# Kernel optimization log

Measured on AMD Instinct MI355X. Metric: run time of the kernel, lower is better.

The kernel has to match this reference:

```python
import jax, jax.numpy as jnp
import numpy as np

EMBED_DIM = 2048
NUM_Q_HEADS = 16
HEAD_DIM = EMBED_DIM // NUM_Q_HEADS  # 128
SCALE = 1.0 / np.sqrt(EMBED_DIM)     # note: module uses 1/sqrt(embed_dim)
B, S = 4, 2048


def setup_inputs() -> dict:
    key = jax.random.key(0)
    ks = jax.random.split(key, 9)
    sd = 0.02
    return {
        "x": jax.random.normal(ks[0], (B, S, EMBED_DIM), dtype=jnp.float32),
        "Wq": jax.random.normal(ks[1], (EMBED_DIM, EMBED_DIM), dtype=jnp.float32) * sd,
        "bq": jnp.zeros((EMBED_DIM,), dtype=jnp.float32),
        "Wk": jax.random.normal(ks[2], (HEAD_DIM, EMBED_DIM), dtype=jnp.float32) * sd,
        "bk": jnp.zeros((HEAD_DIM,), dtype=jnp.float32),
        "Wv": jax.random.normal(ks[3], (HEAD_DIM, EMBED_DIM), dtype=jnp.float32) * sd,
        "bv": jnp.zeros((HEAD_DIM,), dtype=jnp.float32),
        "Wo": jax.random.normal(ks[4], (EMBED_DIM, EMBED_DIM), dtype=jnp.float32) * sd,
        "bo": jnp.zeros((EMBED_DIM,), dtype=jnp.float32),
    }


def reference(x, Wq, bq, Wk, bk, Wv, bv, Wo, bo):
    b, s, _ = x.shape
    # projections (nn.Linear: y = x @ W.T + b)
    q = (x @ Wq.T + bq).reshape(b, s, NUM_Q_HEADS, HEAD_DIM)  # [b,s,h,d]
    k = x @ Wk.T + bk   # [b,t,d] single KV head (MQA)
    v = x @ Wv.T + bv   # [b,t,d]
    # SDPA with single K/V head broadcast across all query heads
    scores = jnp.einsum("bshd,btd->bhst", q, k) * SCALE  # [b,h,s,t]
    attn = jax.nn.softmax(scores, axis=-1)
    out = jnp.einsum("bhst,btd->bshd", attn, v).reshape(b, s, EMBED_DIM)
    return out @ Wo.T + bo
```

## Files before the change

kernel.cpp:

```cpp
#include <hip/hip_runtime.h>
#include <stdint.h>
#include <cmath>

#define B_ 4
#define S_ 2048
#define E_ 2048
#define H_ 16
#define D_ 128
#define M_ (B_*S_)

typedef unsigned short u16;
typedef __attribute__((ext_vector_type(8))) short short8;
typedef __attribute__((ext_vector_type(4))) float f32x4;

__device__ __forceinline__ u16 f2bf(float f) {
  union { float f; uint32_t u; } v; v.f = f;
  uint32_t r = v.u + 0x7fffu + ((v.u >> 16) & 1u);
  return (u16)(r >> 16);
}

__device__ __forceinline__ float exp2_fast(float x) {
  float r; asm("v_exp_f32 %0, %1" : "=v"(r) : "v"(x)); return r;
}

__device__ __forceinline__ uint32_t cvtpk_bf16(float lo, float hi) {
  uint32_t r; asm("v_cvt_pk_bf16_f32 %0, %1, %2" : "=v"(r) : "v"(lo), "v"(hi));
  return r;
}

__device__ __forceinline__ void async16(const void* g, void* s) {
  __builtin_amdgcn_global_load_lds(
      (const __attribute__((address_space(1))) uint32_t*)g,
      (__attribute__((address_space(3))) uint32_t*)s, 16, 0, 0);
}

#define XSEG   4194304L
#define WQSEG  1048576L
#define WKSEG    65536L
__global__ __launch_bounds__(256) void cvt_all(
    const float4* __restrict__ x,  const float4* __restrict__ wq,
    const float4* __restrict__ wk, const float4* __restrict__ wv,
    const float4* __restrict__ wo,
    ushort4* __restrict__ xb,  ushort4* __restrict__ wqb,
    ushort4* __restrict__ wkb, ushort4* __restrict__ wvb,
    ushort4* __restrict__ wob) {
  long i = (long)blockIdx.x * 256 + threadIdx.x;
  const float4* src; ushort4* dst; long off;
  if (i < XSEG)                            { src = x;  dst = xb;  off = 0; }
  else if (i < XSEG + WQSEG)               { src = wq; dst = wqb; off = XSEG; }
  else if (i < XSEG + WQSEG + WKSEG)       { src = wk; dst = wkb; off = XSEG + WQSEG; }
  else if (i < XSEG + WQSEG + 2*WKSEG)     { src = wv; dst = wvb; off = XSEG + WQSEG + WKSEG; }
  else                                     { src = wo; dst = wob; off = XSEG + WQSEG + 2*WKSEG; }
  long j = i - off;
  float4 v = src[j];
  ushort4 o;
  o.x = f2bf(v.x); o.y = f2bf(v.y); o.z = f2bf(v.z); o.w = f2bf(v.w);
  dst[j] = o;
}

template<int OUT>
__global__ __launch_bounds__(512, 2) void gemm256(
    const u16* __restrict__ A, const u16* __restrict__ Bm,
    const float* __restrict__ bias, void* __restrict__ Cout,
    int Ndim, int K, float oscale) {
  __shared__ u16 lA[2][256*64];
  __shared__ u16 lB[2][256*64];
  const int tid = threadIdx.x;
  const int l = tid & 63, w = tid >> 6;
  const int lr = l & 15, lg = l >> 4;
  const int wm = w >> 2, wn = w & 3;
  const int row0A = blockIdx.y * 256;
  const int row0B = blockIdx.x * 256;

  f32x4 acc[8][4] = {};

  auto STAGE = [&](int d, int k0) {
    #pragma unroll
    for (int c = 0; c < 4; ++c) {
      int idx = c*512 + tid;
      int r = idx >> 3, ch = idx & 7;
      async16(A + (size_t)(row0A + r)*K + k0 + (ch ^ (r & 7))*8,
              &lA[d][(size_t)(c*512 + w*64)*8]);
    }
    #pragma unroll
    for (int c = 0; c < 4; ++c) {
      int idx = c*512 + tid;
      int r = idx >> 3, ch = idx & 7;
      async16(Bm + (size_t)(row0B + r)*K + k0 + (ch ^ (r & 7))*8,
              &lB[d][(size_t)(c*512 + w*64)*8]);
    }
  };

  STAGE(0, 0);
  STAGE(1, 64);
  asm volatile("s_waitcnt vmcnt(8)" ::: "memory");
  __builtin_amdgcn_s_barrier();
  asm volatile("" ::: "memory");

  const int nk = K >> 6;
  for (int k = 0; k < nk; ++k) {
    const int d = k & 1;
    const char* bA = (const char*)&lA[d][0];
    const char* bB = (const char*)&lB[d][0];
    short8 afr[8][2], bfr[4][2];

    #pragma unroll
    for (int i = 0; i < 4; ++i)
      #pragma unroll
      for (int ks = 0; ks < 2; ++ks) {
        int ra = wm*128 + i*16 + lr;
        afr[i][ks] = *(const short8*)(bA + ((ra*128 + ks*64 + lg*16) ^ ((ra & 7) << 4)));
      }
    #pragma unroll
    for (int j = 0; j < 2; ++j)
      #pragma unroll
      for (int ks = 0; ks < 2; ++ks) {
        int rb = wn*64 + j*16 + lr;
        bfr[j][ks] = *(const short8*)(bB + ((rb*128 + ks*64 + lg*16) ^ ((rb & 7) << 4)));
      }
    __builtin_amdgcn_s_barrier();
    asm volatile("" ::: "memory");
    __builtin_amdgcn_s_setprio(1);
    #pragma unroll
    for (int i = 0; i < 4; ++i)
      #pragma unroll
      for (int j = 0; j < 2; ++j)
        #pragma unroll
        for (int ks = 0; ks < 2; ++ks)
          acc[i][j] = __builtin_amdgcn_mfma_f32_16x16x32_bf16(
                        afr[i][ks], bfr[j][ks], acc[i][j], 0, 0, 0);
    __builtin_amdgcn_s_setprio(0);
    __builtin_amdgcn_s_barrier();
    asm volatile("" ::: "memory");

    #pragma unroll
    for (int j = 2; j < 4; ++j)
      #pragma unroll
      for (int ks = 0; ks < 2; ++ks) {
        int rb = wn*64 + j*16 + lr;
        bfr[j][ks] = *(const short8*)(bB + ((rb*128 + ks*64 + lg*16) ^ ((rb & 7) << 4)));
      }
    __builtin_amdgcn_s_barrier();
    asm volatile("" ::: "memory");
    __builtin_amdgcn_s_setprio(1);
    #pragma unroll
    for (int i = 0; i < 4; ++i)
      #pragma unroll
      for (int j = 2; j < 4; ++j)
        #pragma unroll
        for (int ks = 0; ks < 2; ++ks)
          acc[i][j] = __builtin_amdgcn_mfma_f32_16x16x32_bf16(
                        afr[i][ks], bfr[j][ks], acc[i][j], 0, 0, 0);
    __builtin_amdgcn_s_setprio(0);
    __builtin_amdgcn_s_barrier();
    asm volatile("" ::: "memory");

    #pragma unroll
    for (int i = 4; i < 8; ++i)
      #pragma unroll
      for (int ks = 0; ks < 2; ++ks) {
        int ra = wm*128 + i*16 + lr;
        afr[i][ks] = *(const short8*)(bA + ((ra*128 + ks*64 + lg*16) ^ ((ra & 7) << 4)));
      }
    __builtin_amdgcn_s_barrier();
    asm volatile("" ::: "memory");
    __builtin_amdgcn_s_setprio(1);
    #pragma unroll
    for (int i = 4; i < 8; ++i)
      #pragma unroll
      for (int j = 0; j < 2; ++j)
        #pragma unroll
        for (int ks = 0; ks < 2; ++ks)
          acc[i][j] = __builtin_amdgcn_mfma_f32_16x16x32_bf16(
                        afr[i][ks], bfr[j][ks], acc[i][j], 0, 0, 0);
    __builtin_amdgcn_s_setprio(0);
    __builtin_amdgcn_s_barrier();
    asm volatile("" ::: "memory");

    bool st = (k + 2 < nk);
    if (st) STAGE(d, (k + 2) << 6);
    __builtin_amdgcn_s_barrier();
    asm volatile("" ::: "memory");
    __builtin_amdgcn_s_setprio(1);
    #pragma unroll
    for (int i = 4; i < 8; ++i)
      #pragma unroll
      for (int j = 2; j < 4; ++j)
        #pragma unroll
        for (int ks = 0; ks < 2; ++ks)
          acc[i][j] = __builtin_amdgcn_mfma_f32_16x16x32_bf16(
                        afr[i][ks], bfr[j][ks], acc[i][j], 0, 0, 0);
    __builtin_amdgcn_s_setprio(0);
    if (st) asm volatile("s_waitcnt vmcnt(8)" ::: "memory");
    else    asm volatile("s_waitcnt vmcnt(0)" ::: "memory");
    __builtin_amdgcn_s_barrier();
    asm volatile("" ::: "memory");
  }

  const int crow0 = row0A + wm*128;
  const int ccol0 = row0B + wn*64;
  #pragma unroll
  for (int j = 0; j < 4; ++j) {
    int col = ccol0 + j*16 + lr;
    float bv = bias[col];
    #pragma unroll
    for (int i = 0; i < 8; ++i) {
      #pragma unroll
      for (int r = 0; r < 4; ++r) {
        int row = crow0 + i*16 + lg*4 + r;
        float vo = (acc[i][j][r] + bv) * oscale;
        if (OUT == 0) ((float*)Cout)[(size_t)row*Ndim + col] = vo;
        else          ((u16*)Cout)[(size_t)row*Ndim + col] = f2bf(vo);
      }
    }
  }
}

__global__ __launch_bounds__(256) void gemm_kv(
    const u16* __restrict__ A, const u16* __restrict__ Wkb, const u16* __restrict__ Wvb,
    const float* __restrict__ bkp, const float* __restrict__ bvp,
    u16* __restrict__ kout, u16* __restrict__ vTout) {
  __shared__ u16 lA[128*64];
  __shared__ u16 lB[128*64];
  const int tid = threadIdx.x;
  const int l = tid & 63, w = tid >> 6;
  const int lr = l & 15, lg = l >> 4;
  const int wr = w >> 1, wc = w & 1;
  const int row0A = blockIdx.y * 128;
  const bool isV = (blockIdx.x != 0);
  const u16* Bm = isV ? Wvb : Wkb;
  const float* bias = isV ? bvp : bkp;

  f32x4 acc[4][4] = {};

  for (int k0 = 0; k0 < E_; k0 += 64) {
    __syncthreads();
    #pragma unroll
    for (int c = 0; c < 4; ++c) {
      int idx = c*256 + tid;
      int r = idx >> 3, ch = idx & 7;
      async16(A + (size_t)(row0A + r)*E_ + k0 + (ch ^ (r & 7))*8,
              lA + (size_t)(c*256 + w*64)*8);
    }
    #pragma unroll
    for (int c = 0; c < 4; ++c) {
      int idx = c*256 + tid;
      int r = idx >> 3, ch = idx & 7;
      async16(Bm + (size_t)r*E_ + k0 + (ch ^ (r & 7))*8,
              lB + (size_t)(c*256 + w*64)*8);
    }
    __syncthreads();
    #pragma unroll
    for (int ks = 0; ks < 2; ++ks) {
      short8 af[4], bfr[4];
      #pragma unroll
      for (int i = 0; i < 4; ++i) {
        int ra = wr*64 + i*16 + lr;
        af[i] = *(const short8*)((const char*)lA +
                 ((ra*128 + ks*64 + lg*16) ^ ((ra & 7) << 4)));
        int rb = wc*64 + i*16 + lr;
        bfr[i] = *(const short8*)((const char*)lB +
                 ((rb*128 + ks*64 + lg*16) ^ ((rb & 7) << 4)));
      }
      #pragma unroll
      for (int i = 0; i < 4; ++i)
        #pragma unroll
        for (int j = 0; j < 4; ++j)
          acc[i][j] = __builtin_amdgcn_mfma_f32_16x16x32_bf16(
                        af[i], bfr[j], acc[i][j], 0, 0, 0);
    }
  }

  const int crow0 = row0A + wr*64;
  #pragma unroll
  for (int j = 0; j < 4; ++j) {
    int col = wc*64 + j*16 + lr;
    float bvv = bias[col];
    #pragma unroll
    for (int i = 0; i < 4; ++i) {
      #pragma unroll
      for (int r = 0; r < 4; ++r) {
        int row = crow0 + i*16 + lg*4 + r;
        float vo = acc[i][j][r] + bvv;
        if (isV) vTout[(size_t)col*M_ + row] = f2bf(vo);
        else     kout[(size_t)row*D_ + col] = f2bf(vo);
      }
    }
  }
}

__global__ __launch_bounds__(512) void mqa_flash(
    const u16* __restrict__ q, const u16* __restrict__ k,
    const u16* __restrict__ vT, u16* __restrict__ o) {
  __shared__ u16 lKbuf[2][64*128];
  __shared__ u16 lVbuf[2][128*64];

  const int tid = threadIdx.x;
  const int l = tid & 63, w = tid >> 6;
  const int lr = l & 15, lg = l >> 4;
  const int qt = blockIdx.x, b = blockIdx.z;
  const int h = blockIdx.y*2 + (w >> 2);
  const int qrow0 = b*S_ + qt*128 + (w & 3)*32;

  short8 qf[2][4];
  #pragma unroll
  for (int st = 0; st < 2; ++st) {
    const u16* qp = q + (size_t)(qrow0 + st*16 + lr)*E_ + h*D_;
    #pragma unroll
    for (int ks = 0; ks < 4; ++ks)
      qf[st][ks] = *(const short8*)(qp + ks*32 + lg*8);
  }

  short8 ones;
  #pragma unroll
  for (int j = 0; j < 8; ++j) ones[j] = (short)0x3F80;

  f32x4 oa[2][8];
  f32x4 la[2] = {f32x4{0.f,0.f,0.f,0.f}, f32x4{0.f,0.f,0.f,0.f}};
  #pragma unroll
  for (int st = 0; st < 2; ++st)
    #pragma unroll
    for (int dn = 0; dn < 8; ++dn) oa[st][dn] = f32x4{0.f,0.f,0.f,0.f};

  const u16* kbase = k + (size_t)b*S_*D_;
  const u16* vbase = vT + (size_t)b*S_;
  char* lK0 = (char*)&lKbuf[0][0];
  char* lV0 = (char*)&lVbuf[0][0];

  auto STAGE = [&](int off, int tt) {
    #pragma unroll
    for (int c = 0; c < 2; ++c) {
      int idx = c*512 + tid;
      int s = idx >> 4, ch = idx & 15;
      int pr = (s & 32) | ((s & 12) << 1) | ((s & 16) >> 2) | (s & 3);
      async16(kbase + (size_t)(tt + pr)*D_ + (ch ^ (s & 7))*8,
              lK0 + off + (size_t)(c*512 + w*64)*16);
    }
    #pragma unroll
    for (int c = 0; c < 2; ++c) {
      int idx = c*512 + tid;
      int r = idx >> 3, ch = idx & 7;
      async16(vbase + (size_t)r*M_ + tt + (ch ^ (r & 7))*8,
              lV0 + off + (size_t)(c*512 + w*64)*16);
    }
  };

  STAGE(0, 0);
  __syncthreads();
  int roff = 0;

  for (int t0 = 0; t0 < S_; t0 += 64) {
    const int woff = roff ^ 16384;
    if (t0 + 64 < S_) STAGE(woff, t0 + 64);

    const char* lKc = lK0 + roff;
    const char* lVc = lV0 + roff;

    f32x4 sa[2][4];
    #pragma unroll
    for (int st = 0; st < 2; ++st)
      #pragma unroll
      for (int n = 0; n < 4; ++n) sa[st][n] = f32x4{0.f,0.f,0.f,0.f};
    __builtin_amdgcn_s_setprio(1);
    #pragma unroll
    for (int n = 0; n < 4; ++n)
      #pragma unroll
      for (int ks = 0; ks < 4; ++ks) {
        short8 kf = *(const short8*)(lKc +
                    (((n*16 + lr)*256 + ks*64 + lg*16) ^ ((lr & 7) << 4)));
        sa[0][n] = __builtin_amdgcn_mfma_f32_16x16x32_bf16(kf, qf[0][ks], sa[0][n], 0, 0, 0);
        sa[1][n] = __builtin_amdgcn_mfma_f32_16x16x32_bf16(kf, qf[1][ks], sa[1][n], 0, 0, 0);
      }
    __builtin_amdgcn_s_setprio(0);

    short8 pa[2][2];
    #pragma unroll
    for (int st = 0; st < 2; ++st) {
      #pragma unroll
      for (int n = 0; n < 4; ++n)
        #pragma unroll
        for (int r = 0; r < 4; ++r)
          sa[st][n][r] = exp2_fast(sa[st][n][r]);
      #pragma unroll
      for (int ks = 0; ks < 2; ++ks) {
        union { short8 s8; uint32_t u[4]; } pu;
        pu.u[0] = cvtpk_bf16(sa[st][2*ks  ][0], sa[st][2*ks  ][1]);
        pu.u[1] = cvtpk_bf16(sa[st][2*ks  ][2], sa[st][2*ks  ][3]);
        pu.u[2] = cvtpk_bf16(sa[st][2*ks+1][0], sa[st][2*ks+1][1]);
        pu.u[3] = cvtpk_bf16(sa[st][2*ks+1][2], sa[st][2*ks+1][3]);
        pa[st][ks] = pu.s8;
      }
    }

    __builtin_amdgcn_s_setprio(1);
    la[0] = __builtin_amdgcn_mfma_f32_16x16x32_bf16(pa[0][0], ones, la[0], 0, 0, 0);
    la[0] = __builtin_amdgcn_mfma_f32_16x16x32_bf16(pa[0][1], ones, la[0], 0, 0, 0);
    la[1] = __builtin_amdgcn_mfma_f32_16x16x32_bf16(pa[1][0], ones, la[1], 0, 0, 0);
    la[1] = __builtin_amdgcn_mfma_f32_16x16x32_bf16(pa[1][1], ones, la[1], 0, 0, 0);

    #pragma unroll
    for (int dn = 0; dn < 8; ++dn)
      #pragma unroll
      for (int ks = 0; ks < 2; ++ks) {
        short8 vf = *(const short8*)(lVc +
                    (((dn*16 + lr)*128 + ks*64 + lg*16) ^ ((lr & 7) << 4)));
        oa[0][dn] = __builtin_amdgcn_mfma_f32_16x16x32_bf16(pa[0][ks], vf, oa[0][dn], 0, 0, 0);
        oa[1][dn] = __builtin_amdgcn_mfma_f32_16x16x32_bf16(pa[1][ks], vf, oa[1][dn], 0, 0, 0);
      }
    __builtin_amdgcn_s_setprio(0);

    __syncthreads();
    roff = woff;
  }

  #pragma unroll
  for (int st = 0; st < 2; ++st) {
    #pragma unroll
    for (int r = 0; r < 4; ++r) {
      float inv = 1.0f / la[st][r];
      u16* orow = o + (size_t)(qrow0 + st*16 + lg*4 + r)*E_ + h*D_ + lr;
      #pragma unroll
      for (int dn = 0; dn < 8; ++dn)
        orow[dn*16] = f2bf(oa[st][dn][r] * inv);
    }
  }
}

extern "C" void kernel_launch(void* const* d_in, const int* in_sizes, int n_in,
                              void* d_out, int out_size, void* d_ws, size_t ws_size,
                              hipStream_t stream) {
  (void)in_sizes; (void)n_in; (void)out_size; (void)ws_size;
  const float* x  = (const float*)d_in[0];
  const float* Wq = (const float*)d_in[1];
  const float* bq = (const float*)d_in[2];
  const float* Wk = (const float*)d_in[3];
  const float* bk = (const float*)d_in[4];
  const float* Wv = (const float*)d_in[5];
  const float* bv = (const float*)d_in[6];
  const float* Wo = (const float*)d_in[7];
  const float* bo = (const float*)d_in[8];
  float* out = (float*)d_out;

  char* ws = (char*)d_ws;
  u16* xb  = (u16*)(ws + 0);
  u16* qb  = (u16*)(ws + 33554432);
  u16* kb  = (u16*)(ws + 67108864);
  u16* vbT = (u16*)(ws + 69206016);
  u16* Wqb = (u16*)(ws + 71303168);
  u16* Wkb = (u16*)(ws + 79691776);
  u16* Wvb = (u16*)(ws + 80216064);
  u16* Wob = (u16*)(ws + 80740352);
  u16* ob  = xb;

  cvt_all<<<25088, 256, 0, stream>>>(
      (const float4*)x, (const float4*)Wq, (const float4*)Wk,
      (const float4*)Wv, (const float4*)Wo,
      (ushort4*)xb, (ushort4*)Wqb, (ushort4*)Wkb, (ushort4*)Wvb, (ushort4*)Wob);

  gemm_kv<<<dim3(2, M_/128), 256, 0, stream>>>(xb, Wkb, Wvb, bk, bv, kb, vbT);

  float qsc = 1.44269504088896f / sqrtf((float)E_);
  gemm256<1><<<dim3(E_/256, M_/256), 512, 0, stream>>>(xb, Wqb, bq, qb, E_, E_, qsc);

  mqa_flash<<<dim3(S_/128, H_/2, B_), 512, 0, stream>>>(qb, kb, vbT, ob);

  gemm256<0><<<dim3(E_/256, M_/256), 512, 0, stream>>>(ob, Wob, bo, out, E_, E_, 1.0f);
}
```

Measured before the change: 367.4 us.

## Split GEMM staging into per-quadrant slots interleaved across MFMA phases and remap blocks per XCD

Restructures the 256x256 GEMM main loop so global-to-LDS loads are issued as four 128-row slots, each placed inside a different MFMA phase. This spreads the memory traffic across the compute phases instead of issuing one burst per k-step. The loop is unrolled by two k-steps with explicit double buffering. It also remaps block IDs so that blocks landing on the same XCD cover neighbouring row and column tiles, to improve L2 reuse. The slot and waitcnt bookkeeping is delicate, and the remap hardcodes an 8-wide grid, which only fits some GEMM shapes.

Measured after the change: 341.8 us. 1.07x faster.

```diff
diff --git a/kernel.cpp b/kernel.cpp
--- a/kernel.cpp
+++ b/kernel.cpp
@@ -63,138 +63,209 @@
     const u16* __restrict__ A, const u16* __restrict__ Bm,
     const float* __restrict__ bias, void* __restrict__ Cout,
     int Ndim, int K, float oscale) {
-  __shared__ u16 lA[2][256*64];
-  __shared__ u16 lB[2][256*64];
+  __shared__ u16 lA[2][2][128*64];
+  __shared__ u16 lB[2][2][128*64];
   const int tid = threadIdx.x;
   const int l = tid & 63, w = tid >> 6;
   const int lr = l & 15, lg = l >> 4;
   const int wm = w >> 2, wn = w & 3;
-  const int row0A = blockIdx.y * 256;
-  const int row0B = blockIdx.x * 256;
+
+  const int bid = blockIdx.y * 8 + blockIdx.x;
+  const int xcd = bid & 7, ii = bid >> 3;
+  const int brow = (xcd >> 1) * 8 + (ii >> 2);
+  const int bcol = (xcd & 1) * 4 + (ii & 3);
+  const int row0A = brow * 256;
+  const int row0B = bcol * 256;
 
   f32x4 acc[8][4] = {};
-
-  auto STAGE = [&](int d, int k0) {
-    #pragma unroll
-    for (int c = 0; c < 4; ++c) {
+  const int nk = K >> 6;
+
+  auto STG = [&](u16* dst, const u16* src, int k0) {
+    #pragma unroll
+    for (int c = 0; c < 2; ++c) {
       int idx = c*512 + tid;
       int r = idx >> 3, ch = idx & 7;
-      async16(A + (size_t)(row0A + r)*K + k0 + (ch ^ (r & 7))*8,
-              &lA[d][(size_t)(c*512 + w*64)*8]);
-    }
-    #pragma unroll
-    for (int c = 0; c < 4; ++c) {
-      int idx = c*512 + tid;
-      int r = idx >> 3, ch = idx & 7;
-      async16(Bm + (size_t)(row0B + r)*K + k0 + (ch ^ (r & 7))*8,
-              &lB[d][(size_t)(c*512 + w*64)*8]);
+      async16(src + (size_t)r*K + k0 + (ch ^ (r & 7))*8,
+              dst + (size_t)(c*512 + w*64)*8);
     }
   };
-
-  STAGE(0, 0);
-  STAGE(1, 64);
-  asm volatile("s_waitcnt vmcnt(8)" ::: "memory");
-  __builtin_amdgcn_s_barrier();
-  asm volatile("" ::: "memory");
-
-  const int nk = K >> 6;
-  for (int k = 0; k < nk; ++k) {
-    const int d = k & 1;
-    const char* bA = (const char*)&lA[d][0];
-    const char* bB = (const char*)&lB[d][0];
-    short8 afr[8][2], bfr[4][2];
-
-    #pragma unroll
-    for (int i = 0; i < 4; ++i)
-      #pragma unroll
-      for (int ks = 0; ks < 2; ++ks) {
-        int ra = wm*128 + i*16 + lr;
-        afr[i][ks] = *(const short8*)(bA + ((ra*128 + ks*64 + lg*16) ^ ((ra & 7) << 4)));
-      }
+  auto SLOT = [&](int t, int s) {
+    if (t >= nk) return;
+    int d = t & 1;
+    if (s < 2) STG(&lA[d][s][0],   A  + (size_t)(row0A + s*128)*K,     t*64);
+    else       STG(&lB[d][s-2][0], Bm + (size_t)(row0B + (s-2)*128)*K, t*64);
+  };
+  auto rdA = [&](int d, int i, int ks) -> short8 {
+    int ra = i*16 + lr;
+    return *(const short8*)((const char*)&lA[d][wm][0] +
+           ((ra*128 + ks*64 + lg*16) ^ ((ra & 7) << 4)));
+  };
+  auto rdB = [&](int d, int j, int ks) -> short8 {
+    int rb = (wn & 1)*64 + j*16 + lr;
+    return *(const short8*)((const char*)&lB[d][wn >> 1][0] +
+           ((rb*128 + ks*64 + lg*16) ^ ((rb & 7) << 4)));
+  };
+  auto BAR = [] { __builtin_amdgcn_s_barrier(); asm volatile("" ::: "memory"); };
+
+  short8 afr[4][2], bfr[4][2];
+
+  SLOT(0, 0); SLOT(0, 1); SLOT(0, 2); SLOT(0, 3);
+  SLOT(1, 0);
+  asm volatile("s_waitcnt vmcnt(2)" ::: "memory");
+  BAR();
+
+  const int niter = nk >> 1;
+  for (int n = 0; n < niter; ++n) {
+    const bool lastit = (n == niter - 1);
+    const int t1 = 2*n + 1;
+
+    #pragma unroll
+    for (int i2 = 0; i2 < 4; ++i2)
+      #pragma unroll
+      for (int ks = 0; ks < 2; ++ks) afr[i2][ks] = rdA(0, i2, ks);
     #pragma unroll
     for (int j = 0; j < 2; ++j)
       #pragma unroll
-      for (int ks = 0; ks < 2; ++ks) {
-        int rb = wn*64 + j*16 + lr;
-        bfr[j][ks] = *(const short8*)(bB + ((rb*128 + ks*64 + lg*16) ^ ((rb & 7) << 4)));
-      }
-    __builtin_amdgcn_s_barrier();
-    asm volatile("" ::: "memory");
-    __builtin_amdgcn_s_setprio(1);
-    #pragma unroll
-    for (int i = 0; i < 4; ++i)
+      for (int ks = 0; ks < 2; ++ks) bfr[j][ks] = rdB(0, j, ks);
+    SLOT(t1, 1);
+    BAR();
+    __builtin_amdgcn_s_setprio(1);
+    #pragma unroll
+    for (int i2 = 0; i2 < 4; ++i2)
       #pragma unroll
       for (int j = 0; j < 2; ++j)
         #pragma unroll
         for (int ks = 0; ks < 2; ++ks)
-          acc[i][j] = __builtin_amdgcn_mfma_f32_16x16x32_bf16(
-                        afr[i][ks], bfr[j][ks], acc[i][j], 0, 0, 0);
-    __builtin_amdgcn_s_setprio(0);
-    __builtin_amdgcn_s_barrier();
-    asm volatile("" ::: "memory");
+          acc[i2][j] = __builtin_amdgcn_mfma_f32_16x16x32_bf16(
+                         afr[i2][ks], bfr[j][ks], acc[i2][j], 0, 0, 0);
+    __builtin_amdgcn_s_setprio(0);
+    BAR();
 
     #pragma unroll
     for (int j = 2; j < 4; ++j)
       #pragma unroll
-      for (int ks = 0; ks < 2; ++ks) {
-        int rb = wn*64 + j*16 + lr;
-        bfr[j][ks] = *(const short8*)(bB + ((rb*128 + ks*64 + lg*16) ^ ((rb & 7) << 4)));
-      }
-    __builtin_amdgcn_s_barrier();
-    asm volatile("" ::: "memory");
-    __builtin_amdgcn_s_setprio(1);
-    #pragma unroll
-    for (int i = 0; i < 4; ++i)
+      for (int ks = 0; ks < 2; ++ks) bfr[j][ks] = rdB(0, j, ks);
+    SLOT(t1, 2);
+    BAR();
+    __builtin_amdgcn_s_setprio(1);
+    #pragma unroll
+    for (int i2 = 0; i2 < 4; ++i2)
       #pragma unroll
       for (int j = 2; j < 4; ++j)
         #pragma unroll
         for (int ks = 0; ks < 2; ++ks)
-          acc[i][j] = __builtin_amdgcn_mfma_f32_16x16x32_bf16(
-                        afr[i][ks], bfr[j][ks], acc[i][j], 0, 0, 0);
-    __builtin_amdgcn_s_setprio(0);
-    __builtin_amdgcn_s_barrier();
-    asm volatile("" ::: "memory");
-
-    #pragma unroll
-    for (int i = 4; i < 8; ++i)
-      #pragma unroll
-      for (int ks = 0; ks < 2; ++ks) {
-        int ra = wm*128 + i*16 + lr;
-        afr[i][ks] = *(const short8*)(bA + ((ra*128 + ks*64 + lg*16) ^ ((ra & 7) << 4)));
-      }
-    __builtin_amdgcn_s_barrier();
-    asm volatile("" ::: "memory");
-    __builtin_amdgcn_s_setprio(1);
-    #pragma unroll
-    for (int i = 4; i < 8; ++i)
+          acc[i2][j] = __builtin_amdgcn_mfma_f32_16x16x32_bf16(
+                         afr[i2][ks], bfr[j][ks], acc[i2][j], 0, 0, 0);
+    __builtin_amdgcn_s_setprio(0);
+    BAR();
+
+    #pragma unroll
+    for (int i2 = 0; i2 < 4; ++i2)
+      #pragma unroll
+      for (int ks = 0; ks < 2; ++ks) afr[i2][ks] = rdA(0, 4 + i2, ks);
+    SLOT(t1, 3);
+    BAR();
+    __builtin_amdgcn_s_setprio(1);
+    #pragma unroll
+    for (int i2 = 0; i2 < 4; ++i2)
       #pragma unroll
       for (int j = 0; j < 2; ++j)
         #pragma unroll
         for (int ks = 0; ks < 2; ++ks)
-          acc[i][j] = __builtin_amdgcn_mfma_f32_16x16x32_bf16(
-                        afr[i][ks], bfr[j][ks], acc[i][j], 0, 0, 0);
-    __builtin_amdgcn_s_setprio(0);
-    __builtin_amdgcn_s_barrier();
-    asm volatile("" ::: "memory");
-
-    bool st = (k + 2 < nk);
-    if (st) STAGE(d, (k + 2) << 6);
-    __builtin_amdgcn_s_barrier();
-    asm volatile("" ::: "memory");
-    __builtin_amdgcn_s_setprio(1);
-    #pragma unroll
-    for (int i = 4; i < 8; ++i)
+          acc[4 + i2][j] = __builtin_amdgcn_mfma_f32_16x16x32_bf16(
+                             afr[i2][ks], bfr[j][ks], acc[4 + i2][j], 0, 0, 0);
+    __builtin_amdgcn_s_setprio(0);
+    BAR();
+
+    SLOT(2*n + 2, 0);
+    BAR();
+    __builtin_amdgcn_s_setprio(1);
+    #pragma unroll
+    for (int i2 = 0; i2 < 4; ++i2)
       #pragma unroll
       for (int j = 2; j < 4; ++j)
         #pragma unroll
         for (int ks = 0; ks < 2; ++ks)
-          acc[i][j] = __builtin_amdgcn_mfma_f32_16x16x32_bf16(
-                        afr[i][ks], bfr[j][ks], acc[i][j], 0, 0, 0);
-    __builtin_amdgcn_s_setprio(0);
-    if (st) asm volatile("s_waitcnt vmcnt(8)" ::: "memory");
-    else    asm volatile("s_waitcnt vmcnt(0)" ::: "memory");
-    __builtin_amdgcn_s_barrier();
-    asm volatile("" ::: "memory");
+          acc[4 + i2][j] = __builtin_amdgcn_mfma_f32_16x16x32_bf16(
+                             afr[i2][ks], bfr[j][ks], acc[4 + i2][j], 0, 0, 0);
+    __builtin_amdgcn_s_setprio(0);
+    if (lastit) asm volatile("s_waitcnt vmcnt(0)" ::: "memory");
+    else        asm volatile("s_waitcnt vmcnt(2)" ::: "memory");
+    BAR();
+
+    #pragma unroll
+    for (int i2 = 0; i2 < 4; ++i2)
+      #pragma unroll
+      for (int ks = 0; ks < 2; ++ks) afr[i2][ks] = rdA(1, i2, ks);
+    #pragma unroll
+    for (int j = 0; j < 2; ++j)
+      #pragma unroll
+      for (int ks = 0; ks < 2; ++ks) bfr[j][ks] = rdB(1, j, ks);
+    SLOT(2*n + 2, 1);
+    BAR();
+    __builtin_amdgcn_s_setprio(1);
+    #pragma unroll
+    for (int i2 = 0; i2 < 4; ++i2)
+      #pragma unroll
+      for (int j = 0; j < 2; ++j)
+        #pragma unroll
+        for (int ks = 0; ks < 2; ++ks)
+          acc[i2][j] = __builtin_amdgcn_mfma_f32_16x16x32_bf16(
+                         afr[i2][ks], bfr[j][ks], acc[i2][j], 0, 0, 0);
+    __builtin_amdgcn_s_setprio(0);
+    BAR();
+
+    #pragma unroll
+    for (int j = 2; j < 4; ++j)
+      #pragma unroll
+      for (int ks = 0; ks < 2; ++ks) bfr[j][ks] = rdB(1, j, ks);
+    SLOT(2*n + 2, 2);
+    BAR();
+    __builtin_amdgcn_s_setprio(1);
+    #pragma unroll
+    for (int i2 = 0; i2 < 4; ++i2)
+      #pragma unroll
+      for (int j = 2; j < 4; ++j)
+        #pragma unroll
+        for (int ks = 0; ks < 2; ++ks)
+          acc[i2][j] = __builtin_amdgcn_mfma_f32_16x16x32_bf16(
+                         afr[i2][ks], bfr[j][ks], acc[i2][j], 0, 0, 0);
+    __builtin_amdgcn_s_setprio(0);
+    BAR();
+
+    #pragma unroll
+    for (int i2 = 0; i2 < 4; ++i2)
+      #pragma unroll
+      for (int ks = 0; ks < 2; ++ks) afr[i2][ks] = rdA(1, 4 + i2, ks);
+    SLOT(2*n + 2, 3);
+    BAR();
+    __builtin_amdgcn_s_setprio(1);
+    #pragma unroll
+    for (int i2 = 0; i2 < 4; ++i2)
+      #pragma unroll
+      for (int j = 0; j < 2; ++j)
+        #pragma unroll
+        for (int ks = 0; ks < 2; ++ks)
+          acc[4 + i2][j] = __builtin_amdgcn_mfma_f32_16x16x32_bf16(
+                             afr[i2][ks], bfr[j][ks], acc[4 + i2][j], 0, 0, 0);
+    __builtin_amdgcn_s_setprio(0);
+    BAR();
+
+    SLOT(2*n + 3, 0);
+    BAR();
+    __builtin_amdgcn_s_setprio(1);
+    #pragma unroll
+    for (int i2 = 0; i2 < 4; ++i2)
+      #pragma unroll
+      for (int j = 2; j < 4; ++j)
+        #pragma unroll
+        for (int ks = 0; ks < 2; ++ks)
+          acc[4 + i2][j] = __builtin_amdgcn_mfma_f32_16x16x32_bf16(
+                             afr[i2][ks], bfr[j][ks], acc[4 + i2][j], 0, 0, 0);
+    __builtin_amdgcn_s_setprio(0);
+    if (lastit) asm volatile("s_waitcnt vmcnt(0)" ::: "memory");
+    else        asm volatile("s_waitcnt vmcnt(2)" ::: "memory");
+    BAR();
   }
 
   const int crow0 = row0A + wm*128;
```
